# Kernel optimization log

Hardware: AMD Instinct MI355X
Metric: run time of the kernel (lower is better)

## Reference

```python
import jax, jax.numpy as jnp
from jax import lax
import numpy as np

IN_DIM, HID, B, T = 8, 50, 4096, 512

def setup_inputs() -> dict:
    key = jax.random.key(0)
    ks = jax.random.split(key, 8)
    s_ih = 1.0 / np.sqrt(HID)
    return {
        "x": jax.random.normal(ks[0], (B, T, IN_DIM), dtype=jnp.float32),
        "W_ih": jax.random.uniform(ks[1], (3 * HID, IN_DIM), jnp.float32, -s_ih, s_ih),
        "W_hh": jax.random.uniform(ks[2], (3 * HID, HID), jnp.float32, -s_ih, s_ih),
        "b_ih": jax.random.uniform(ks[3], (3 * HID,), jnp.float32, -s_ih, s_ih),
        "b_hh": jax.random.uniform(ks[4], (3 * HID,), jnp.float32, -s_ih, s_ih),
        "W_out": jax.random.uniform(ks[5], (1, HID), jnp.float32, -s_ih, s_ih),
        "b_out": jax.random.uniform(ks[6], (1,), jnp.float32, -s_ih, s_ih),
    }

def reference(x, W_ih, W_hh, b_ih, b_hh, W_out, b_out):
    # Precompute input projections for all timesteps: [B, T, 3H]
    xW = jnp.einsum('bti,gi->btg', x, W_ih) + b_ih

    def step(h, xw_t):  # h: [B, H], xw_t: [B, 3H]
        gi_r, gi_z, gi_n = jnp.split(xw_t, 3, axis=-1)
        gh = h @ W_hh.T + b_hh
        gh_r, gh_z, gh_n = jnp.split(gh, 3, axis=-1)
        r = jax.nn.sigmoid(gi_r + gh_r)
        z = jax.nn.sigmoid(gi_z + gh_z)
        n = jnp.tanh(gi_n + r * gh_n)
        h_new = (1.0 - z) * n + z * h
        return h_new, None

    h0 = jnp.zeros((x.shape[0], W_hh.shape[1]), dtype=x.dtype)
    hT, _ = lax.scan(step, h0, jnp.moveaxis(xW, 1, 0))  # scan over time
    # Linear head on final hidden state; torch squeezes the layer dim -> [B, 1]
    return hT @ W_out.T + b_out
```

## Files before the change

### kernel.cpp

```cpp
#include <hip/hip_runtime.h>

#define HID 50
#define IND 8
#define TLEN 512
#define NB 16
#define CH 128
#define XSTR 1032
#define BSTR 72
#define NTHR 512

typedef _Float16 f16x8 __attribute__((ext_vector_type(8)));
typedef _Float16 f16x4 __attribute__((ext_vector_type(4)));
typedef float f32x4 __attribute__((ext_vector_type(4)));

__device__ __forceinline__ float fast_sigmoid(float v) {
    float e = __builtin_amdgcn_exp2f(-1.44269504f * v);
    return __builtin_amdgcn_rcpf(1.0f + e);
}
__device__ __forceinline__ float fast_tanh(float v) {
    float e = __builtin_amdgcn_exp2f(2.88539008f * v);
    return 1.0f - 2.0f * __builtin_amdgcn_rcpf(e + 1.0f);
}

__global__ __launch_bounds__(NTHR, 1) void gru_mfma7(
    const float* __restrict__ x,
    const float* __restrict__ W_ih,
    const float* __restrict__ W_hh,
    const float* __restrict__ b_ih,
    const float* __restrict__ b_hh,
    const float* __restrict__ W_out,
    const float* __restrict__ b_out,
    float* __restrict__ out)
{
    const int tid  = threadIdx.x;
    const int wave = tid >> 6;
    const int lane = tid & 63;
    const int m16  = lane & 15;
    const int quad = lane >> 4;
    const int bb   = blockIdx.x;

    const int t0  = 2 * wave;
    const int t1  = 2 * wave + 1;
    const int jh0 = 4 * t0 + quad;
    const int jh1 = 4 * t1 + quad;

    __shared__ _Float16 x_lds[NB * XSTR];
    __shared__ _Float16 B_lds[2][16 * BSTR];
    __shared__ float    red[NB * 56];

    auto aval = [&](int tt, int k) -> float {
        const int R  = 16 * tt + m16;
        const int rj = R >> 2;
        const int g  = R & 3;
        if (rj >= HID) return 0.f;
        if (g <= 1) {
            if (k < HID) return W_hh[(g * HID + rj) * HID + k];
            if (k >= 56) return W_ih[(g * HID + rj) * IND + (k - 56)];
            return 0.f;
        }
        if (g == 2) return (k < HID) ? W_hh[(2 * HID + rj) * HID + k] : 0.f;
        return (k >= 56) ? W_ih[(2 * HID + rj) * IND + (k - 56)] : 0.f;
    };

    f16x8 a00, a01, a10, a11;
#pragma unroll
    for (int j = 0; j < 8; ++j) {
        a00[j] = (_Float16)aval(t0, quad * 8 + j);
        a01[j] = (_Float16)aval(t0, 32 + quad * 8 + j);
        a10[j] = (_Float16)aval(t1, quad * 8 + j);
        a11[j] = (_Float16)aval(t1, 32 + quad * 8 + j);
    }

    auto mkbias = [&](int jh) -> f32x4 {
        f32x4 b = {0.f, 0.f, 0.f, 0.f};
        if (jh < HID) {
            b[0] = b_ih[jh] + b_hh[jh];
            b[1] = b_ih[HID + jh] + b_hh[HID + jh];
            b[2] = b_hh[2 * HID + jh];
            b[3] = b_ih[2 * HID + jh];
        }
        return b;
    };
    const f32x4 bias0 = mkbias(jh0);
    const f32x4 bias1 = mkbias(jh1);

    float h0 = 0.f, h1 = 0.f;

    auto stage_chunk = [&](int c) {
        const int n = tid >> 5;
        const int s = tid & 31;
        const float4* src = (const float4*)(x + ((size_t)(bb * NB + n) * TLEN + (size_t)c * CH) * IND);
#pragma unroll
        for (int r2 = 0; r2 < 8; ++r2) {
            const int fidx = s + 32 * r2;
            const float4 v = src[fidx];
            const int trel = fidx >> 1;
            const int d    = (fidx & 1) * 4;
            *(f16x4*)&x_lds[n * XSTR + trel * 8 + d] =
                f16x4{(_Float16)v.x, (_Float16)v.y, (_Float16)v.z, (_Float16)v.w};
        }
    };

    {
        _Float16* bz = &B_lds[0][0];
        for (int idx = tid; idx < 2 * 16 * BSTR; idx += NTHR)
            bz[idx] = (_Float16)0.f;
    }
    stage_chunk(0);
    __syncthreads();

    const int bq = m16 * BSTR + quad * 8;
    const int bw = m16 * BSTR;

    auto gates = [&](const f32x4& cc, float h) -> float {
        const float r = fast_sigmoid(cc[0]);
        const float z = fast_sigmoid(cc[1]);
        const float n = fast_tanh(cc[3] + r * cc[2]);
        return n + z * (h - n);
    };

    for (int c = 0; c < 4; ++c) {
        if (c != 0) { stage_chunk(c); __syncthreads(); }
        const _Float16* xb = &x_lds[m16 * XSTR];
        for (int i = 0; i < CH; i += 2) {
            {
                const f16x8 bf0 = *(const f16x8*)&B_lds[0][bq];
                const f16x8 bf1 = (quad == 3) ? *(const f16x8*)(xb + (size_t)i * 8)
                                              : *(const f16x8*)&B_lds[0][bq + 32];
                f32x4 c0 = __builtin_amdgcn_mfma_f32_16x16x32_f16(a00, bf0, bias0, 0, 0, 0);
                f32x4 c1 = __builtin_amdgcn_mfma_f32_16x16x32_f16(a10, bf0, bias1, 0, 0, 0);
                c0 = __builtin_amdgcn_mfma_f32_16x16x32_f16(a01, bf1, c0, 0, 0, 0);
                c1 = __builtin_amdgcn_mfma_f32_16x16x32_f16(a11, bf1, c1, 0, 0, 0);
                h0 = gates(c0, h0);
                h1 = gates(c1, h1);
                B_lds[1][bw + jh0] = (_Float16)h0;
                B_lds[1][bw + jh1] = (_Float16)h1;
                __syncthreads();
            }
            {
                const f16x8 bf0 = *(const f16x8*)&B_lds[1][bq];
                const f16x8 bf1 = (quad == 3) ? *(const f16x8*)(xb + (size_t)(i + 1) * 8)
                                              : *(const f16x8*)&B_lds[1][bq + 32];
                f32x4 c0 = __builtin_amdgcn_mfma_f32_16x16x32_f16(a00, bf0, bias0, 0, 0, 0);
                f32x4 c1 = __builtin_amdgcn_mfma_f32_16x16x32_f16(a10, bf0, bias1, 0, 0, 0);
                c0 = __builtin_amdgcn_mfma_f32_16x16x32_f16(a01, bf1, c0, 0, 0, 0);
                c1 = __builtin_amdgcn_mfma_f32_16x16x32_f16(a11, bf1, c1, 0, 0, 0);
                h0 = gates(c0, h0);
                h1 = gates(c1, h1);
                B_lds[0][bw + jh0] = (_Float16)h0;
                B_lds[0][bw + jh1] = (_Float16)h1;
                __syncthreads();
            }
        }
    }

    if (jh0 < HID) red[m16 * 56 + jh0] = h0 * W_out[jh0];
    if (jh1 < HID) red[m16 * 56 + jh1] = h1 * W_out[jh1];
    __syncthreads();
    if (tid < NB) {
        float s = b_out[0];
        for (int j = 0; j < HID; ++j) s += red[tid * 56 + j];
        out[bb * NB + tid] = s;
    }
}

extern "C" void kernel_launch(void* const* d_in, const int* in_sizes, int n_in,
                              void* d_out, int out_size, void* d_ws, size_t ws_size,
                              hipStream_t stream) {
    const float* x     = (const float*)d_in[0];
    const float* W_ih  = (const float*)d_in[1];
    const float* W_hh  = (const float*)d_in[2];
    const float* b_ih  = (const float*)d_in[3];
    const float* b_hh  = (const float*)d_in[4];
    const float* W_out = (const float*)d_in[5];
    const float* b_out = (const float*)d_in[6];
    float* out = (float*)d_out;

    const int B = in_sizes[0] / (TLEN * IND);
    gru_mfma7<<<B / NB, NTHR, 0, stream>>>(x, W_ih, W_hh, b_ih, b_hh, W_out, b_out, out);
}
```

Measured before the change: 249.3 us.

## Fold exp2 scaling into weights, merge gate reciprocals, dedicate idle wave to x copy

The log2(e) scale factors are folded into the f16 weight fragments and the biases, so the MFMA outputs feed exp2 directly. The z/n blend is rewritten as one rational expression that needs a single reciprocal instead of three. Wave 7, whose rows are all padding, now copies each timestep's x into the B operand buffer, so the compute waves no longer do a quad-dependent select between x_lds and B_lds. The goal is a shorter serial per-step chain. In exchange, the merged formula can overflow to inf/NaN at large pre-activations, and scaling the weights before the f16 conversion changes rounding.

Measured after the change: 242.1 us. 2.9% less time.

```diff
diff --git a/kernel.cpp b/kernel.cpp
--- a/kernel.cpp
+++ b/kernel.cpp
@@ -13,16 +13,7 @@
 typedef _Float16 f16x4 __attribute__((ext_vector_type(4)));
 typedef float f32x4 __attribute__((ext_vector_type(4)));
 
-__device__ __forceinline__ float fast_sigmoid(float v) {
-    float e = __builtin_amdgcn_exp2f(-1.44269504f * v);
-    return __builtin_amdgcn_rcpf(1.0f + e);
-}
-__device__ __forceinline__ float fast_tanh(float v) {
-    float e = __builtin_amdgcn_exp2f(2.88539008f * v);
-    return 1.0f - 2.0f * __builtin_amdgcn_rcpf(e + 1.0f);
-}
-
-__global__ __launch_bounds__(NTHR, 1) void gru_mfma7(
+__global__ __launch_bounds__(NTHR, 1) void gru_mfma8(
     const float* __restrict__ x,
     const float* __restrict__ W_ih,
     const float* __restrict__ W_hh,
@@ -53,13 +44,17 @@
         const int rj = R >> 2;
         const int g  = R & 3;
         if (rj >= HID) return 0.f;
+        const float sc = (g <= 1) ? -1.44269504f : 2.88539008f;
+        float w = 0.f;
         if (g <= 1) {
-            if (k < HID) return W_hh[(g * HID + rj) * HID + k];
-            if (k >= 56) return W_ih[(g * HID + rj) * IND + (k - 56)];
-            return 0.f;
+            if (k < HID)      w = W_hh[(g * HID + rj) * HID + k];
+            else if (k >= 56) w = W_ih[(g * HID + rj) * IND + (k - 56)];
+        } else if (g == 2) {
+            if (k < HID)      w = W_hh[(2 * HID + rj) * HID + k];
+        } else {
+            if (k >= 56)      w = W_ih[(2 * HID + rj) * IND + (k - 56)];
         }
-        if (g == 2) return (k < HID) ? W_hh[(2 * HID + rj) * HID + k] : 0.f;
-        return (k >= 56) ? W_ih[(2 * HID + rj) * IND + (k - 56)] : 0.f;
+        return sc * w;
     };
 
     f16x8 a00, a01, a10, a11;
@@ -74,10 +69,10 @@
     auto mkbias = [&](int jh) -> f32x4 {
         f32x4 b = {0.f, 0.f, 0.f, 0.f};
         if (jh < HID) {
-            b[0] = b_ih[jh] + b_hh[jh];
-            b[1] = b_ih[HID + jh] + b_hh[HID + jh];
-            b[2] = b_hh[2 * HID + jh];
-            b[3] = b_ih[2 * HID + jh];
+            b[0] = -1.44269504f * (b_ih[jh] + b_hh[jh]);
+            b[1] = -1.44269504f * (b_ih[HID + jh] + b_hh[HID + jh]);
+            b[2] =  2.88539008f * b_hh[2 * HID + jh];
+            b[3] =  2.88539008f * b_ih[2 * HID + jh];
         }
         return b;
     };
@@ -101,6 +96,11 @@
         }
     };
 
+    auto copy_x = [&](int trel, int buf) {
+        *(unsigned*)&B_lds[buf][m16 * BSTR + 56 + 2 * quad] =
+            *(const unsigned*)&x_lds[m16 * XSTR + trel * 8 + 2 * quad];
+    };
+
     {
         _Float16* bz = &B_lds[0][0];
         for (int idx = tid; idx < 2 * 16 * BSTR; idx += NTHR)
@@ -113,20 +113,26 @@
     const int bw = m16 * BSTR;
 
     auto gates = [&](const f32x4& cc, float h) -> float {
-        const float r = fast_sigmoid(cc[0]);
-        const float z = fast_sigmoid(cc[1]);
-        const float n = fast_tanh(cc[3] + r * cc[2]);
-        return n + z * (h - n);
+        const float R2 = __builtin_amdgcn_exp2f(cc[0]);
+        const float r  = __builtin_amdgcn_rcpf(1.0f + R2);
+        const float Z2 = __builtin_amdgcn_exp2f(cc[1]);
+        const float E  = __builtin_amdgcn_exp2f(cc[3] + r * cc[2]);
+        const float num = E * (Z2 + h) + (h - Z2);
+        const float den = (E + 1.0f) * (Z2 + 1.0f);
+        return num * __builtin_amdgcn_rcpf(den);
     };
 
     for (int c = 0; c < 4; ++c) {
         if (c != 0) { stage_chunk(c); __syncthreads(); }
-        const _Float16* xb = &x_lds[m16 * XSTR];
+        if (wave == 7) copy_x(0, 0);
+        __syncthreads();
+#pragma unroll 4
         for (int i = 0; i < CH; i += 2) {
-            {
+            if (wave == 7) {
+                copy_x(i + 1, 1);
+            } else {
                 const f16x8 bf0 = *(const f16x8*)&B_lds[0][bq];
-                const f16x8 bf1 = (quad == 3) ? *(const f16x8*)(xb + (size_t)i * 8)
-                                              : *(const f16x8*)&B_lds[0][bq + 32];
+                const f16x8 bf1 = *(const f16x8*)&B_lds[0][bq + 32];
                 f32x4 c0 = __builtin_amdgcn_mfma_f32_16x16x32_f16(a00, bf0, bias0, 0, 0, 0);
                 f32x4 c1 = __builtin_amdgcn_mfma_f32_16x16x32_f16(a10, bf0, bias1, 0, 0, 0);
                 c0 = __builtin_amdgcn_mfma_f32_16x16x32_f16(a01, bf1, c0, 0, 0, 0);
@@ -135,12 +141,13 @@
                 h1 = gates(c1, h1);
                 B_lds[1][bw + jh0] = (_Float16)h0;
                 B_lds[1][bw + jh1] = (_Float16)h1;
-                __syncthreads();
             }
-            {
+            __syncthreads();
+            if (wave == 7) {
+                if (i + 2 < CH) copy_x(i + 2, 0);
+            } else {
                 const f16x8 bf0 = *(const f16x8*)&B_lds[1][bq];
-                const f16x8 bf1 = (quad == 3) ? *(const f16x8*)(xb + (size_t)(i + 1) * 8)
-                                              : *(const f16x8*)&B_lds[1][bq + 32];
+                const f16x8 bf1 = *(const f16x8*)&B_lds[1][bq + 32];
                 f32x4 c0 = __builtin_amdgcn_mfma_f32_16x16x32_f16(a00, bf0, bias0, 0, 0, 0);
                 f32x4 c1 = __builtin_amdgcn_mfma_f32_16x16x32_f16(a10, bf0, bias1, 0, 0, 0);
                 c0 = __builtin_amdgcn_mfma_f32_16x16x32_f16(a01, bf1, c0, 0, 0, 0);
@@ -149,8 +156,8 @@
                 h1 = gates(c1, h1);
                 B_lds[0][bw + jh0] = (_Float16)h0;
                 B_lds[0][bw + jh1] = (_Float16)h1;
-                __syncthreads();
             }
+            __syncthreads();
         }
     }
 
@@ -177,5 +184,5 @@
     float* out = (float*)d_out;
 
     const int B = in_sizes[0] / (TLEN * IND);
-    gru_mfma7<<<B / NB, NTHR, 0, stream>>>(x, W_ih, W_hh, b_ih, b_hh, W_out, b_out, out);
+    gru_mfma8<<<B / NB, NTHR, 0, stream>>>(x, W_ih, W_hh, b_ih, b_hh, W_out, b_out, out);
 }
```
